# Kernel tuning notes

Hardware: AMD Instinct MI355X
Metric: run time of the kernel (lower is better)

The kernel has to match this reference:

```python
import jax, jax.numpy as jnp
import numpy as np

N_NODES = 50000
N_EDGES = 800000
EDGE_DIM = 16
EMB = 128
BN_EPS = 1e-5


def setup_inputs() -> dict:
    key = jax.random.key(0)
    ks = jax.random.split(key, 8)
    node_feats = jax.random.normal(ks[0], (N_NODES, EMB), jnp.float32)
    edge_feats = jax.random.normal(ks[1], (N_EDGES, EDGE_DIM), jnp.float32)
    src = jax.random.randint(ks[2], (N_EDGES,), 0, N_NODES, dtype=jnp.int32)
    dst = jax.random.randint(ks[3], (N_EDGES,), 0, N_NODES, dtype=jnp.int32)
    def kaiming(k, shape, fan_in):
        return (jax.random.normal(k, shape, jnp.float32) / np.float32(np.sqrt(fan_in)))
    W_edge = kaiming(ks[4], (EDGE_DIM, EMB), EDGE_DIM)
    b_edge = jnp.zeros((EMB,), jnp.float32)
    W1 = kaiming(ks[5], (EMB, 2 * EMB), EMB)
    b1 = jnp.zeros((2 * EMB,), jnp.float32)
    W2 = kaiming(ks[6], (2 * EMB, EMB), 2 * EMB)
    b2 = jnp.zeros((EMB,), jnp.float32)
    bn_gamma = jnp.ones((EMB,), jnp.float32)
    bn_beta = jnp.zeros((EMB,), jnp.float32)
    return dict(node_feats=node_feats, edge_feats=edge_feats, W_edge=W_edge,
                b_edge=b_edge, W1=W1, b1=b1, W2=W2, b2=b2,
                bn_gamma=bn_gamma, bn_beta=bn_beta, src=src, dst=dst)


def reference(node_feats, edge_feats, W_edge, b_edge, W1, b1, W2, b2,
              bn_gamma, bn_beta, src, dst):
    n_nodes = node_feats.shape[0]
    # edge embedding: Linear(num_edge_emb -> emb_dim)
    edge_embeds = edge_feats @ W_edge + b_edge            # [E, D]
    # u_add_e message: gather source node feats, add edge embeds
    msg = node_feats[src] + edge_embeds                   # [E, D]
    # sum aggregation to destination nodes
    agg = jax.ops.segment_sum(msg, dst, num_segments=n_nodes)  # [N, D]
    # MLP: Linear(D, 2D) -> ReLU -> Linear(2D, D)
    h = jax.nn.relu(agg @ W1 + b1) @ W2 + b2              # [N, D]
    # BatchNorm1d over the node (batch) dim, training-mode batch stats
    mean = jnp.mean(h, axis=0)
    var = jnp.mean((h - mean) ** 2, axis=0)               # biased variance
    out = (h - mean) * jax.lax.rsqrt(var + BN_EPS) * bn_gamma + bn_beta
    return out
```

## Files before the change

kernel.cpp:

```cpp
#include <hip/hip_runtime.h>
#include <stdint.h>

#define NN 50000
#define NE 800000
#define NB_MLP ((NN + 63) / 64)
#define NSB ((NN + 255) / 256)

typedef unsigned int u32;
typedef unsigned short u16;
typedef __attribute__((ext_vector_type(8))) short short8;
typedef __attribute__((ext_vector_type(4))) float f32x4;
typedef int int4u __attribute__((ext_vector_type(4), aligned(4)));
typedef int int2u __attribute__((ext_vector_type(2), aligned(4)));

__device__ __align__(16) u16   g_nf16[NN * 128];
__device__ __align__(16) u16   g_agg16[NN * 128];
__device__ __align__(16) float g_h[NN * 128];
__device__ __align__(16) float g_We[16 * 128];
__device__ __align__(16) float g_be[128];
__device__ __align__(16) float g_b1[256];
__device__ __align__(16) float g_b2[128];
__device__ __align__(16) float g_gamma[128];
__device__ __align__(16) float g_beta[128];
__device__ __align__(16) u16   g_W1p[128 * 256];
__device__ __align__(16) u16   g_W2p[256 * 128];
__device__ __align__(16) int   g_rowptr[NN + 1];
__device__ __align__(16) int   g_blocksum[NSB];
__device__ __align__(16) int2  g_es[NE];

__device__ __align__(16) int   g_zero[2 * NN + 256];
#define g_deg    (g_zero)
#define g_cursor (g_zero + NN)
#define g_stats  ((float*)(g_zero + 2 * NN))

__device__ __forceinline__ float bf2f(u16 u) {
  return __uint_as_float(((u32)u) << 16);
}
__device__ __forceinline__ u16 f2bf(float x) {
  u32 u = __float_as_uint(x);
  u32 r = (u + 0x7fffu + ((u >> 16) & 1u)) >> 16;
  return (u16)r;
}
__device__ __forceinline__ bool is_bf16(const u32* probe) {
  return probe[0] == 0x3F803F80u;
}

__global__ void k_prep(const int* __restrict__ dst, int E, const void* nodep,
                       const void* We, const void* be, const void* W1,
                       const void* b1, const void* W2, const void* b2,
                       const void* ga, const void* bt, const u32* probe) {
  const bool b16 = is_bf16(probe);
  const int gid = blockIdx.x * blockDim.x + threadIdx.x;
  const int stride = gridDim.x * blockDim.x;
  for (int e = gid; e < E; e += stride) atomicAdd(&g_deg[dst[e]], 1);
  if (!b16) {
    const float2* s = (const float2*)nodep;
    u32* d = (u32*)g_nf16;
    for (int i = gid; i < NN * 64; i += stride) {
      float2 v = s[i];
      d[i] = (u32)f2bf(v.x) | ((u32)f2bf(v.y) << 16);
    }
  }
  const int i = gid;
  if (i < 2816) {
    const void* s; float* d; int off;
    if      (i < 2048) { s = We; d = g_We;    off = i; }
    else if (i < 2176) { s = be; d = g_be;    off = i - 2048; }
    else if (i < 2432) { s = b1; d = g_b1;    off = i - 2176; }
    else if (i < 2560) { s = b2; d = g_b2;    off = i - 2432; }
    else if (i < 2688) { s = ga; d = g_gamma; off = i - 2560; }
    else               { s = bt; d = g_beta;  off = i - 2688; }
    d[off] = b16 ? bf2f(((const u16*)s)[off]) : ((const float*)s)[off];
  } else if (i < 35584) {
    const int idx = i - 2816;
    const int j = idx & 7, lane = (idx >> 3) & 63, nt = (idx >> 9) & 15, kt = idx >> 13;
    const int k = kt * 32 + (lane >> 4) * 8 + j;
    const int n = nt * 16 + (lane & 15);
    g_W1p[idx] = b16 ? ((const u16*)W1)[k * 256 + n]
                     : f2bf(((const float*)W1)[k * 256 + n]);
  } else if (i < 68352) {
    const int idx = i - 35584;
    const int j = idx & 7, lane = (idx >> 3) & 63, nt = (idx >> 9) & 7, kt = idx >> 12;
    const int k = kt * 32 + (lane >> 4) * 8 + j;
    const int n = nt * 16 + (lane & 15);
    g_W2p[idx] = b16 ? ((const u16*)W2)[k * 128 + n]
                     : f2bf(((const float*)W2)[k * 128 + n]);
  }
}

__global__ __launch_bounds__(256) void scan1_kernel() {
  __shared__ int s[256];
  const int t = threadIdx.x;
  const int i = blockIdx.x * 256 + t;
  int v = (i < NN) ? g_deg[i] : 0;
  s[t] = v;
  __syncthreads();
#pragma unroll
  for (int off = 1; off < 256; off <<= 1) {
    int x = (t >= off) ? s[t - off] : 0;
    __syncthreads();
    s[t] += x;
    __syncthreads();
  }
  if (i < NN) g_rowptr[i] = s[t] - v;
  if (t == 255) g_blocksum[blockIdx.x] = s[255];
}

__global__ __launch_bounds__(256) void scan2_kernel(int E) {
  __shared__ int s[256];
  const int t = threadIdx.x;
  int v = (t < NSB) ? g_blocksum[t] : 0;
  s[t] = v;
  __syncthreads();
#pragma unroll
  for (int off = 1; off < 256; off <<= 1) {
    int x = (t >= off) ? s[t - off] : 0;
    __syncthreads();
    s[t] += x;
    __syncthreads();
  }
  if (t < NSB) g_blocksum[t] = s[t] - v;
  if (t == 0) g_rowptr[NN] = E;
}

__global__ __launch_bounds__(256) void scatter_kernel(const int* __restrict__ src,
                                                      const int* __restrict__ dst, int E) {
  const int e = blockIdx.x * blockDim.x + threadIdx.x;
  if (e >= E) return;
  const int d = dst[e];
  const int p = g_rowptr[d] + g_blocksum[d >> 8] + atomicAdd(&g_cursor[d], 1);
  g_es[p] = make_int2(e, src[e]);
}

__device__ __forceinline__ void accum8(float* acc, uint4 v) {
  const u32 vv[4] = {v.x, v.y, v.z, v.w};
#pragma unroll
  for (int q = 0; q < 4; ++q) {
    acc[2 * q]     += bf2f((u16)vv[q]);
    acc[2 * q + 1] += bf2f((u16)(vv[q] >> 16));
  }
}
template <bool B16>
__device__ __forceinline__ float ef_at(const void* efin, size_t idx) {
  if constexpr (B16) return bf2f(((const u16*)efin)[idx]);
  else               return ((const float*)efin)[idx];
}
template <bool B16>
__device__ __forceinline__ void agg_body(const u16* __restrict__ nf,
                                         const void* __restrict__ efin) {
  const int tid  = threadIdx.x;
  const int wv   = tid >> 6;
  const int lane = tid & 63;
  const int g    = lane >> 4;
  const int i16  = lane & 15;
  const int t    = blockIdx.x * 4 + wv;
  if (t >= NN) return;
  const int j0 = g_rowptr[t] + g_blocksum[t >> 8];
  const int j1 = (t + 1 == NN) ? g_rowptr[NN]
                               : (g_rowptr[t + 1] + g_blocksum[(t + 1) >> 8]);
  const int d0 = i16 * 8;

  float acc[8];
#pragma unroll
  for (int q = 0; q < 8; ++q) acc[q] = 0.f;
  float sEF = 0.f;

  int j = j0;
  for (; j + 15 < j1; j += 16) {
    const int* ep = (const int*)g_es + 2 * (j + 4 * g);
    int4u ea = *(const int4u*)ep;
    int4u eb = *(const int4u*)(ep + 4);
    uint4 v0 = *(const uint4*)(nf + (size_t)ea.y * 128 + d0);
    uint4 v1 = *(const uint4*)(nf + (size_t)ea.w * 128 + d0);
    uint4 v2 = *(const uint4*)(nf + (size_t)eb.y * 128 + d0);
    uint4 v3 = *(const uint4*)(nf + (size_t)eb.w * 128 + d0);
    float f0 = ef_at<B16>(efin, (size_t)ea.x * 16 + i16);
    float f1 = ef_at<B16>(efin, (size_t)ea.z * 16 + i16);
    float f2 = ef_at<B16>(efin, (size_t)eb.x * 16 + i16);
    float f3 = ef_at<B16>(efin, (size_t)eb.z * 16 + i16);
    accum8(acc, v0);
    accum8(acc, v1);
    accum8(acc, v2);
    accum8(acc, v3);
    sEF += (f0 + f1) + (f2 + f3);
  }
  for (; j + 3 < j1; j += 4) {
    int2u p = *(const int2u*)((const int*)g_es + 2 * (j + g));
    uint4 v = *(const uint4*)(nf + (size_t)p.y * 128 + d0);
    float fe = ef_at<B16>(efin, (size_t)p.x * 16 + i16);
    accum8(acc, v);
    sEF += fe;
  }
  if (j + g < j1) {
    int2u p = *(const int2u*)((const int*)g_es + 2 * (j + g));
    uint4 v = *(const uint4*)(nf + (size_t)p.y * 128 + d0);
    float fe = ef_at<B16>(efin, (size_t)p.x * 16 + i16);
    accum8(acc, v);
    sEF += fe;
  }

  sEF += __shfl_xor(sEF, 16, 64);
  sEF += __shfl_xor(sEF, 32, 64);

#pragma unroll
  for (int kk = 0; kk < 4; ++kk) {
    const int k = g * 4 + kk;
    const float ek = __shfl(sEF, k, 16);
#pragma unroll
    for (int q = 0; q < 8; ++q)
      acc[q] = fmaf(ek, g_We[k * 128 + d0 + q], acc[q]);
  }
  if (g == 0) {
    const float deg = (float)(j1 - j0);
#pragma unroll
    for (int q = 0; q < 8; ++q)
      acc[q] = fmaf(deg, g_be[d0 + q], acc[q]);
  }

#pragma unroll
  for (int q = 0; q < 8; ++q) {
    acc[q] += __shfl_xor(acc[q], 16, 64);
    acc[q] += __shfl_xor(acc[q], 32, 64);
  }

  if (g == 0) {
    uint4 o;
    o.x = (u32)f2bf(acc[0]) | ((u32)f2bf(acc[1]) << 16);
    o.y = (u32)f2bf(acc[2]) | ((u32)f2bf(acc[3]) << 16);
    o.z = (u32)f2bf(acc[4]) | ((u32)f2bf(acc[5]) << 16);
    o.w = (u32)f2bf(acc[6]) | ((u32)f2bf(acc[7]) << 16);
    *(uint4*)(g_agg16 + (size_t)t * 128 + d0) = o;
  }
}
__global__ __launch_bounds__(256) void agg_kernel(const void* nfin, const void* efin,
                                                  const u32* probe) {
  if (is_bf16(probe)) agg_body<true>((const u16*)nfin, efin);
  else                agg_body<false>(g_nf16, efin);
}

__global__ __launch_bounds__(256, 4) void mlp_mfma(int N) {
  __shared__ u16 sT[2 * 64 * 136];
  __shared__ float sb1[256];
  __shared__ float sb2[128];
  __shared__ float sStat[256];

  const int tid  = threadIdx.x;
  const int w    = tid >> 6;
  const int lane = tid & 63;
  const int quad = lane >> 4;
  const int l15  = lane & 15;
  const int row0 = blockIdx.x * 64;

  sb1[tid] = g_b1[tid];
  if (tid < 128) sb2[tid] = g_b2[tid];
  sStat[tid] = 0.f;

#pragma unroll
  for (int i = 0; i < 4; ++i) {
    int lin = i * 256 + tid;
    int r = lin >> 4, seg = lin & 15;
    uint4 v = make_uint4(0u, 0u, 0u, 0u);
    if (row0 + r < N)
      v = *(const uint4*)(g_agg16 + ((size_t)(row0 + r) * 128 + seg * 8));
    *(uint4*)(sT + r * 136 + seg * 8) = v;
  }
  __syncthreads();

  f32x4 acc[2][4];

#pragma unroll
  for (int p = 0; p < 2; ++p) {
    const int ntb = (p == 0) ? (8 + 2 * w) : (2 * w);
#pragma unroll
    for (int nti = 0; nti < 2; ++nti)
#pragma unroll
      for (int m = 0; m < 4; ++m)
        acc[nti][m] = (f32x4){0.f, 0.f, 0.f, 0.f};
#pragma unroll
    for (int kt = 0; kt < 4; ++kt) {
      short8 a[4];
#pragma unroll
      for (int m = 0; m < 4; ++m)
        a[m] = *(const short8*)(sT + (m * 16 + l15) * 136 + kt * 32 + quad * 8);
#pragma unroll
      for (int nti = 0; nti < 2; ++nti) {
        short8 b = *(const short8*)(g_W1p + ((kt * 16 + ntb + nti) * 64 + lane) * 8);
#pragma unroll
        for (int m = 0; m < 4; ++m)
          acc[nti][m] = __builtin_amdgcn_mfma_f32_16x16x32_bf16(a[m], b, acc[nti][m], 0, 0, 0);
      }
    }
    if (p == 1) __syncthreads();
    u16* dstT = (p == 0) ? (sT + 8704) : sT;
    const int cb = (p == 0) ? (ntb - 8) * 16 : ntb * 16;
#pragma unroll
    for (int nti = 0; nti < 2; ++nti) {
      float bias = sb1[(ntb + nti) * 16 + l15];
#pragma unroll
      for (int m = 0; m < 4; ++m)
#pragma unroll
        for (int reg = 0; reg < 4; ++reg) {
          float v = acc[nti][m][reg] + bias;
          v = v > 0.f ? v : 0.f;
          dstT[(m * 16 + quad * 4 + reg) * 136 + cb + nti * 16 + l15] = f2bf(v);
        }
    }
  }
  __syncthreads();

#pragma unroll
  for (int nti = 0; nti < 2; ++nti)
#pragma unroll
    for (int m = 0; m < 4; ++m)
      acc[nti][m] = (f32x4){0.f, 0.f, 0.f, 0.f};
#pragma unroll
  for (int kt = 0; kt < 8; ++kt) {
    const u16* srcT = (kt < 4) ? sT : (sT + 8704);
    const int kc = (kt & 3) * 32 + quad * 8;
    short8 a[4];
#pragma unroll
    for (int m = 0; m < 4; ++m)
      a[m] = *(const short8*)(srcT + (m * 16 + l15) * 136 + kc);
#pragma unroll
    for (int nti = 0; nti < 2; ++nti) {
      short8 b = *(const short8*)(g_W2p + ((kt * 8 + 2 * w + nti) * 64 + lane) * 8);
#pragma unroll
      for (int m = 0; m < 4; ++m)
        acc[nti][m] = __builtin_amdgcn_mfma_f32_16x16x32_bf16(a[m], b, acc[nti][m], 0, 0, 0);
    }
  }

#pragma unroll
  for (int nti = 0; nti < 2; ++nti) {
    const int col = (2 * w + nti) * 16 + l15;
    const float bias = sb2[col];
    float ss = 0.f, sq = 0.f;
#pragma unroll
    for (int m = 0; m < 4; ++m)
#pragma unroll
      for (int reg = 0; reg < 4; ++reg) {
        const int row = row0 + m * 16 + quad * 4 + reg;
        if (row < N) {
          float hv = acc[nti][m][reg] + bias;
          g_h[(size_t)row * 128 + col] = hv;
          ss += hv;
          sq += hv * hv;
        }
      }
    atomicAdd(&sStat[col], ss);
    atomicAdd(&sStat[128 + col], sq);
  }
  __syncthreads();
  atomicAdd(&g_stats[tid], sStat[tid]);
}

__global__ void bn_kernel(const u32* probe, void* outp, int N) {
  const bool b16 = is_bf16(probe);
  const float invN = 1.0f / (float)N;
  int i = blockIdx.x * blockDim.x + threadIdx.x;
  const int total = N * 32;
  const int stride = gridDim.x * blockDim.x;
  for (; i < total; i += stride) {
    int c4 = (i & 31) * 4;
    float4 hv = ((const float4*)g_h)[i];
    float in[4] = {hv.x, hv.y, hv.z, hv.w};
    float o[4];
#pragma unroll
    for (int j = 0; j < 4; ++j) {
      int c = c4 + j;
      float mean = g_stats[c] * invN;
      float var  = g_stats[128 + c] * invN - mean * mean;
      float sc   = rsqrtf(var + 1e-5f) * g_gamma[c];
      o[j] = (in[j] - mean) * sc + g_beta[c];
    }
    if (b16) {
      ((ushort4*)outp)[i] = make_ushort4(f2bf(o[0]), f2bf(o[1]), f2bf(o[2]), f2bf(o[3]));
    } else {
      ((float4*)outp)[i] = make_float4(o[0], o[1], o[2], o[3]);
    }
  }
}

extern "C" void kernel_launch(void* const* d_in, const int* in_sizes, int n_in,
                              void* d_out, int out_size, void* d_ws, size_t ws_size,
                              hipStream_t stream) {
  const int N = in_sizes[0] / 128;
  const int E = in_sizes[10];
  const u32* probe = (const u32*)d_in[8];
  const int* src = (const int*)d_in[10];
  const int* dst = (const int*)d_in[11];

  static void* zp = nullptr;
  if (!zp) hipGetSymbolAddress(&zp, HIP_SYMBOL(g_zero));
  hipMemsetAsync(zp, 0, (2 * NN + 256) * sizeof(int), stream);

  hipLaunchKernelGGL(k_prep, dim3(1024), dim3(256), 0, stream,
                     dst, E, d_in[0], d_in[2], d_in[3], d_in[4], d_in[5],
                     d_in[6], d_in[7], d_in[8], d_in[9], probe);
  hipLaunchKernelGGL(scan1_kernel, dim3(NSB), dim3(256), 0, stream);
  hipLaunchKernelGGL(scan2_kernel, dim3(1), dim3(256), 0, stream, E);
  const int ebl = (E + 255) / 256;
  hipLaunchKernelGGL(scatter_kernel, dim3(ebl), dim3(256), 0, stream, src, dst, E);
  hipLaunchKernelGGL(agg_kernel, dim3((NN + 3) / 4), dim3(256), 0, stream,
                     d_in[0], d_in[1], probe);
  hipLaunchKernelGGL(mlp_mfma, dim3(NB_MLP), dim3(256), 0, stream, N);
  hipLaunchKernelGGL(bn_kernel, dim3(2048), dim3(256), 0, stream,
                     probe, d_out, N);
}
```

Before: 321.1 us.

## Pre-aggregate edge features with atomics in prep; CSR stores only source ids

Edge features are now summed per destination node in the prep kernel using 12.8M float atomicAdds into a new zeroed buffer, so the aggregation kernel no longer gathers edge features per edge. The CSR array shrinks from (edge id, src) pairs to src only, and each wave's four lane groups now take contiguous edge ranges using vectorized int4 loads. The cost moves to a large volume of scattered atomics and a bigger memset. Summation order also becomes nondeterministic.

```diff
diff --git a/kernel.cpp b/kernel.cpp
--- a/kernel.cpp
+++ b/kernel.cpp
@@ -11,7 +11,6 @@
 typedef __attribute__((ext_vector_type(8))) short short8;
 typedef __attribute__((ext_vector_type(4))) float f32x4;
 typedef int int4u __attribute__((ext_vector_type(4), aligned(4)));
-typedef int int2u __attribute__((ext_vector_type(2), aligned(4)));
 
 __device__ __align__(16) u16   g_nf16[NN * 128];
 __device__ __align__(16) u16   g_agg16[NN * 128];
@@ -26,12 +25,13 @@
 __device__ __align__(16) u16   g_W2p[256 * 128];
 __device__ __align__(16) int   g_rowptr[NN + 1];
 __device__ __align__(16) int   g_blocksum[NSB];
-__device__ __align__(16) int2  g_es[NE];
-
-__device__ __align__(16) int   g_zero[2 * NN + 256];
+__device__ __align__(16) int   g_src[NE];
+
+__device__ __align__(16) int   g_zero[2 * NN + 256 + NN * 16];
 #define g_deg    (g_zero)
 #define g_cursor (g_zero + NN)
 #define g_stats  ((float*)(g_zero + 2 * NN))
+#define g_aggE   ((float*)(g_zero + 2 * NN + 256))
 
 __device__ __forceinline__ float bf2f(u16 u) {
   return __uint_as_float(((u32)u) << 16);
@@ -46,6 +46,7 @@
 }
 
 __global__ void k_prep(const int* __restrict__ dst, int E, const void* nodep,
+                       const void* efp,
                        const void* We, const void* be, const void* W1,
                        const void* b1, const void* W2, const void* b2,
                        const void* ga, const void* bt, const u32* probe) {
@@ -53,6 +54,11 @@
   const int gid = blockIdx.x * blockDim.x + threadIdx.x;
   const int stride = gridDim.x * blockDim.x;
   for (int e = gid; e < E; e += stride) atomicAdd(&g_deg[dst[e]], 1);
+  for (int x = gid; x < E * 16; x += stride) {
+    const int e = x >> 4, k = x & 15;
+    const float v = b16 ? bf2f(((const u16*)efp)[x]) : ((const float*)efp)[x];
+    atomicAdd(&g_aggE[(size_t)dst[e] * 16 + k], v);
+  }
   if (!b16) {
     const float2* s = (const float2*)nodep;
     u32* d = (u32*)g_nf16;
@@ -129,7 +135,7 @@
   if (e >= E) return;
   const int d = dst[e];
   const int p = g_rowptr[d] + g_blocksum[d >> 8] + atomicAdd(&g_cursor[d], 1);
-  g_es[p] = make_int2(e, src[e]);
+  g_src[p] = src[e];
 }
 
 __device__ __forceinline__ void accum8(float* acc, uint4 v) {
@@ -140,14 +146,8 @@
     acc[2 * q + 1] += bf2f((u16)(vv[q] >> 16));
   }
 }
-template <bool B16>
-__device__ __forceinline__ float ef_at(const void* efin, size_t idx) {
-  if constexpr (B16) return bf2f(((const u16*)efin)[idx]);
-  else               return ((const float*)efin)[idx];
-}
-template <bool B16>
-__device__ __forceinline__ void agg_body(const u16* __restrict__ nf,
-                                         const void* __restrict__ efin) {
+__global__ __launch_bounds__(256) void agg_kernel(const void* nfin, const u32* probe) {
+  const u16* __restrict__ nf = is_bf16(probe) ? (const u16*)nfin : g_nf16;
   const int tid  = threadIdx.x;
   const int wv   = tid >> 6;
   const int lane = tid & 63;
@@ -158,63 +158,57 @@
   const int j0 = g_rowptr[t] + g_blocksum[t >> 8];
   const int j1 = (t + 1 == NN) ? g_rowptr[NN]
                                : (g_rowptr[t + 1] + g_blocksum[(t + 1) >> 8]);
+  const int deg = j1 - j0;
   const int d0 = i16 * 8;
 
+  const int q4 = deg >> 2, r4 = deg & 3;
+  const int gs = j0 + g * q4 + (g < r4 ? g : r4);
+  const int ge = gs + q4 + (g < r4 ? 1 : 0);
+
   float acc[8];
 #pragma unroll
   for (int q = 0; q < 8; ++q) acc[q] = 0.f;
-  float sEF = 0.f;
-
-  int j = j0;
-  for (; j + 15 < j1; j += 16) {
-    const int* ep = (const int*)g_es + 2 * (j + 4 * g);
-    int4u ea = *(const int4u*)ep;
-    int4u eb = *(const int4u*)(ep + 4);
-    uint4 v0 = *(const uint4*)(nf + (size_t)ea.y * 128 + d0);
-    uint4 v1 = *(const uint4*)(nf + (size_t)ea.w * 128 + d0);
-    uint4 v2 = *(const uint4*)(nf + (size_t)eb.y * 128 + d0);
-    uint4 v3 = *(const uint4*)(nf + (size_t)eb.w * 128 + d0);
-    float f0 = ef_at<B16>(efin, (size_t)ea.x * 16 + i16);
-    float f1 = ef_at<B16>(efin, (size_t)ea.z * 16 + i16);
-    float f2 = ef_at<B16>(efin, (size_t)eb.x * 16 + i16);
-    float f3 = ef_at<B16>(efin, (size_t)eb.z * 16 + i16);
+
+  int jj = gs;
+  for (; jj + 3 < ge; jj += 4) {
+    int4u s4 = *(const int4u*)(g_src + jj);
+    uint4 v0 = *(const uint4*)(nf + (size_t)s4.x * 128 + d0);
+    uint4 v1 = *(const uint4*)(nf + (size_t)s4.y * 128 + d0);
+    uint4 v2 = *(const uint4*)(nf + (size_t)s4.z * 128 + d0);
+    uint4 v3 = *(const uint4*)(nf + (size_t)s4.w * 128 + d0);
     accum8(acc, v0);
     accum8(acc, v1);
     accum8(acc, v2);
     accum8(acc, v3);
-    sEF += (f0 + f1) + (f2 + f3);
-  }
-  for (; j + 3 < j1; j += 4) {
-    int2u p = *(const int2u*)((const int*)g_es + 2 * (j + g));
-    uint4 v = *(const uint4*)(nf + (size_t)p.y * 128 + d0);
-    float fe = ef_at<B16>(efin, (size_t)p.x * 16 + i16);
-    accum8(acc, v);
-    sEF += fe;
-  }
-  if (j + g < j1) {
-    int2u p = *(const int2u*)((const int*)g_es + 2 * (j + g));
-    uint4 v = *(const uint4*)(nf + (size_t)p.y * 128 + d0);
-    float fe = ef_at<B16>(efin, (size_t)p.x * 16 + i16);
-    accum8(acc, v);
-    sEF += fe;
-  }
-
-  sEF += __shfl_xor(sEF, 16, 64);
-  sEF += __shfl_xor(sEF, 32, 64);
+  }
+  const int rem = ge - jj;
+  if (rem > 0) {
+    const int s0 = g_src[jj];
+    const int s1 = (rem > 1) ? g_src[jj + 1] : s0;
+    const int s2 = (rem > 2) ? g_src[jj + 2] : s0;
+    uint4 v0 = *(const uint4*)(nf + (size_t)s0 * 128 + d0);
+    uint4 v1 = *(const uint4*)(nf + (size_t)s1 * 128 + d0);
+    uint4 v2 = *(const uint4*)(nf + (size_t)s2 * 128 + d0);
+    accum8(acc, v0);
+    if (rem > 1) accum8(acc, v1);
+    if (rem > 2) accum8(acc, v2);
+  }
+
+  const float aE = g_aggE[(size_t)t * 16 + i16];
 
 #pragma unroll
   for (int kk = 0; kk < 4; ++kk) {
     const int k = g * 4 + kk;
-    const float ek = __shfl(sEF, k, 16);
+    const float ek = __shfl(aE, k, 16);
 #pragma unroll
     for (int q = 0; q < 8; ++q)
       acc[q] = fmaf(ek, g_We[k * 128 + d0 + q], acc[q]);
   }
   if (g == 0) {
-    const float deg = (float)(j1 - j0);
+    const float degf = (float)deg;
 #pragma unroll
     for (int q = 0; q < 8; ++q)
-      acc[q] = fmaf(deg, g_be[d0 + q], acc[q]);
+      acc[q] = fmaf(degf, g_be[d0 + q], acc[q]);
   }
 
 #pragma unroll
@@ -231,11 +225,6 @@
     o.w = (u32)f2bf(acc[6]) | ((u32)f2bf(acc[7]) << 16);
     *(uint4*)(g_agg16 + (size_t)t * 128 + d0) = o;
   }
-}
-__global__ __launch_bounds__(256) void agg_kernel(const void* nfin, const void* efin,
-                                                  const u32* probe) {
-  if (is_bf16(probe)) agg_body<true>((const u16*)nfin, efin);
-  else                agg_body<false>(g_nf16, efin);
 }
 
 __global__ __launch_bounds__(256, 4) void mlp_mfma(int N) {
@@ -392,17 +381,17 @@
 
   static void* zp = nullptr;
   if (!zp) hipGetSymbolAddress(&zp, HIP_SYMBOL(g_zero));
-  hipMemsetAsync(zp, 0, (2 * NN + 256) * sizeof(int), stream);
-
-  hipLaunchKernelGGL(k_prep, dim3(1024), dim3(256), 0, stream,
-                     dst, E, d_in[0], d_in[2], d_in[3], d_in[4], d_in[5],
-                     d_in[6], d_in[7], d_in[8], d_in[9], probe);
+  hipMemsetAsync(zp, 0, (2 * NN + 256 + NN * 16) * sizeof(int), stream);
+
+  hipLaunchKernelGGL(k_prep, dim3(2048), dim3(256), 0, stream,
+                     dst, E, d_in[0], d_in[1], d_in[2], d_in[3], d_in[4],
+                     d_in[5], d_in[6], d_in[7], d_in[8], d_in[9], probe);
   hipLaunchKernelGGL(scan1_kernel, dim3(NSB), dim3(256), 0, stream);
   hipLaunchKernelGGL(scan2_kernel, dim3(1), dim3(256), 0, stream, E);
   const int ebl = (E + 255) / 256;
   hipLaunchKernelGGL(scatter_kernel, dim3(ebl), dim3(256), 0, stream, src, dst, E);
   hipLaunchKernelGGL(agg_kernel, dim3((NN + 3) / 4), dim3(256), 0, stream,
-                     d_in[0], d_in[1], probe);
+                     d_in[0], probe);
   hipLaunchKernelGGL(mlp_mfma, dim3(NB_MLP), dim3(256), 0, stream, N);
   hipLaunchKernelGGL(bn_kernel, dim3(2048), dim3(256), 0, stream,
                      probe, d_out, N);
```

New measurement: 375.6 us. 1.17x slower.
